# Kernel tuning notes

Hardware: AMD Instinct MI355X
Metric: run time of the kernel (lower is better)

The kernel has to match this reference:

```python
import jax, jax.numpy as jnp
import numpy as np

V, D, H, KVH, L, T_SEQ = 32000, 768, 12, 4, 6, 1024
HD = D // H          # 64
KVD = KVH * HD       # 256
B = 2
VE_LAYERS = [1, 3, 5]                 # has_ve(i, 6): i % 2 == 1
WINDOWS = [T_SEQ // 2, T_SEQ, T_SEQ // 2, T_SEQ, T_SEQ // 2, T_SEQ]  # 'SL' pattern, last forced L
SOFTCAP = 15.0


def _norm(x):
    # RMSNorm without learned scale, eps=1e-6, computed in fp32
    xf = x.astype(jnp.float32)
    return (xf * jax.lax.rsqrt(jnp.mean(jnp.square(xf), axis=-1, keepdims=True) + 1e-6)).astype(x.dtype)


def _rope(x, cos, sin):
    d = x.shape[3] // 2
    x1, x2 = x[..., :d], x[..., d:]
    return jnp.concatenate([x1 * cos + x2 * sin, -x1 * sin + x2 * cos], axis=3)


def _rotary_tables(T):
    ch = jnp.arange(0, HD, 2, dtype=jnp.float32)
    inv_freq = 1.0 / (10000.0 ** (ch / HD))
    t = jnp.arange(T, dtype=jnp.float32)
    freqs = jnp.outer(t, inv_freq)                 # [T, HD/2]
    cos = jnp.cos(freqs)[None, :, None, :]         # [1, T, 1, HD/2]
    sin = jnp.sin(freqs)[None, :, None, :]
    return cos, sin


def setup_inputs() -> dict:
    key = jax.random.key(0)
    ks = jax.random.split(key, 12)
    s = 0.02
    return {
        "idx": jax.random.randint(ks[0], (B, T_SEQ), 0, V, dtype=jnp.int64) if jax.config.read('jax_enable_x64') else jax.random.randint(ks[0], (B, T_SEQ), 0, V),
        "wte": jax.random.normal(ks[1], (V, D), jnp.float32) * s,
        "Wq": jax.random.normal(ks[2], (L, D, D), jnp.float32) * s,
        "Wk": jax.random.normal(ks[3], (L, KVD, D), jnp.float32) * s,
        "Wv": jax.random.normal(ks[4], (L, KVD, D), jnp.float32) * s,
        "Wo": jax.random.normal(ks[5], (L, D, D), jnp.float32) * s,
        "Wfc": jax.random.normal(ks[6], (L, 4 * D, D), jnp.float32) * s,
        "Wproj": jax.random.normal(ks[7], (L, D, 4 * D), jnp.float32) * s,
        "ve_tables": jax.random.normal(ks[8], (len(VE_LAYERS), V, KVD), jnp.float32) * s,
        "ve_gates": jax.random.normal(ks[9], (len(VE_LAYERS), KVH, 32), jnp.float32) * s,
        "resid_lambdas": jnp.ones((L,), jnp.float32),
        "x0_lambdas": jnp.zeros((L,), jnp.float32),
        "lm_head_w": jax.random.normal(ks[10], (V, D), jnp.float32) * s,
    }


def _attn(xn, idx, i, Wq, Wk, Wv, Wo, ve_tables, ve_gates, cos, sin, pos):
    Bsz, T, _ = xn.shape
    q = jnp.einsum('btc,dc->btd', xn, Wq[i]).reshape(Bsz, T, H, HD)
    k = jnp.einsum('btc,dc->btd', xn, Wk[i]).reshape(Bsz, T, KVH, HD)
    v = jnp.einsum('btc,dc->btd', xn, Wv[i]).reshape(Bsz, T, KVH, HD)
    if i in VE_LAYERS:
        j = VE_LAYERS.index(i)
        ve = ve_tables[j][idx].reshape(Bsz, T, KVH, HD)
        gate = 2.0 * jax.nn.sigmoid(jnp.einsum('btc,hc->bth', xn[..., :32], ve_gates[j]))
        v = v + gate[..., None] * ve
    q = _norm(_rope(q, cos, sin))
    k = _norm(_rope(k, cos, sin))
    # [B, heads, T, HD]
    q = q.transpose(0, 2, 1, 3)
    k = jnp.repeat(k.transpose(0, 2, 1, 3), H // KVH, axis=1)
    v = jnp.repeat(v.transpose(0, 2, 1, 3), H // KVH, axis=1)
    scores = jnp.einsum('bhqd,bhkd->bhqk', q, k) / np.sqrt(HD).astype(np.float32)
    w = WINDOWS[i]
    diff = pos[:, None] - pos[None, :]             # query - key
    mask = (diff >= 0) & (diff < w)                # w==T => plain causal
    scores = jnp.where(mask[None, None], scores, -jnp.inf)
    attn = jax.nn.softmax(scores, axis=-1)
    y = jnp.einsum('bhqk,bhkd->bhqd', attn, v)
    y = y.transpose(0, 2, 1, 3).reshape(Bsz, T, D)
    return jnp.einsum('btd,cd->btc', y, Wo[i])


def reference(idx, wte, Wq, Wk, Wv, Wo, Wfc, Wproj, ve_tables, ve_gates,
              resid_lambdas, x0_lambdas, lm_head_w):
    T = idx.shape[1]
    cos, sin = _rotary_tables(T)
    pos = jnp.arange(T)
    x = _norm(wte[idx])                            # [B, T, D]
    x0 = x
    for i in range(L):
        x = resid_lambdas[i] * x + x0_lambdas[i] * x0
        xn = _norm(x)
        x = x + _attn(xn, idx, i, Wq, Wk, Wv, Wo, ve_tables, ve_gates, cos, sin, pos)
        xn2 = _norm(x)
        h = jnp.square(jax.nn.relu(jnp.einsum('btc,fc->btf', xn2, Wfc[i])))
        x = x + jnp.einsum('btf,cf->btc', h, Wproj[i])
    x = _norm(x)
    logits = jnp.einsum('btd,vd->btv', x, lm_head_w).astype(jnp.float32)
    return SOFTCAP * jnp.tanh(logits / SOFTCAP)
```

## Files before the change

### kernel.cpp

```cpp
#include <hip/hip_runtime.h>
#include <math.h>

#define V_SZ   32000
#define D_SZ   768
#define H_N    12
#define KVH_N  4
#define L_N    6
#define T_SEQ  1024
#define HD_SZ  64
#define KVD_SZ 256
#define B_SZ   2
#define M_TOK  (B_SZ * T_SEQ)

typedef unsigned int u32;
typedef unsigned short u16;
typedef float f32x4 __attribute__((ext_vector_type(4)));
typedef short bf16x8 __attribute__((ext_vector_type(8)));
typedef u32 u32x4 __attribute__((ext_vector_type(4)));

__device__ __forceinline__ float block_reduce_sum_256(float v, float* ws4) {
#pragma unroll
  for (int o = 32; o; o >>= 1) v += __shfl_xor(v, o, 64);
  int wid = threadIdx.x >> 6;
  if ((threadIdx.x & 63) == 0) ws4[wid] = v;
  __syncthreads();
  return ws4[0] + ws4[1] + ws4[2] + ws4[3];
}

__global__ __launch_bounds__(256) void embed_norm_k(
    const int* __restrict__ idx, const float* __restrict__ wte,
    float* __restrict__ x, float* __restrict__ x0) {
  __shared__ float ws4[4];
  int bt = blockIdx.x;
  int tok = idx[bt];
  const float* row = wte + (size_t)tok * D_SZ;
  float v[3]; float ss = 0.f;
#pragma unroll
  for (int i = 0; i < 3; i++) { v[i] = row[threadIdx.x + i * 256]; ss += v[i] * v[i]; }
  ss = block_reduce_sum_256(ss, ws4);
  float r = rsqrtf(ss * (1.f / D_SZ) + 1e-6f);
  size_t base = (size_t)bt * D_SZ + threadIdx.x;
#pragma unroll
  for (int i = 0; i < 3; i++) {
    float o = v[i] * r;
    x[base + i * 256] = o;
    x0[base + i * 256] = o;
  }
}

__global__ __launch_bounds__(256) void resid_norm_k(
    float* __restrict__ x, const float* __restrict__ x0, float* __restrict__ xn,
    const float* __restrict__ rl, const float* __restrict__ xl, int layer) {
  __shared__ float ws4[4];
  int bt = blockIdx.x;
  float a = 1.f, b = 0.f;
  if (layer >= 0) { a = rl[layer]; b = xl[layer]; }
  size_t base = (size_t)bt * D_SZ + threadIdx.x;
  float v[3]; float ss = 0.f;
#pragma unroll
  for (int i = 0; i < 3; i++) {
    float nv = a * x[base + i * 256] + b * x0[base + i * 256];
    v[i] = nv; ss += nv * nv;
    if (layer >= 0) x[base + i * 256] = nv;
  }
  ss = block_reduce_sum_256(ss, ws4);
  float r = rsqrtf(ss * (1.f / D_SZ) + 1e-6f);
#pragma unroll
  for (int i = 0; i < 3; i++) xn[base + i * 256] = v[i] * r;
}

__global__ __launch_bounds__(64) void rope_norm_k(float* __restrict__ q, float* __restrict__ k) {
  int bt = blockIdx.x;
  int slot = blockIdx.y;
  int t = bt & (T_SEQ - 1);
  float* p;
  if (slot < H_N) p = q + (size_t)bt * D_SZ + slot * HD_SZ;
  else            p = k + (size_t)bt * KVD_SZ + (slot - H_N) * HD_SZ;
  int d = threadIdx.x;
  float self = p[d];
  float partner = p[d ^ 32];
  int j = d & 31;
  float inv = powf(10000.f, -(float)(2 * j) * (1.f / HD_SZ));
  float ang = (float)t * inv;
  float c = cosf(ang), s = sinf(ang);
  float out = (d < 32) ? (self * c + partner * s) : (self * c - partner * s);
  float ss = out * out;
#pragma unroll
  for (int o = 32; o; o >>= 1) ss += __shfl_xor(ss, o, 64);
  float r = rsqrtf(ss * (1.f / HD_SZ) + 1e-6f);
  p[d] = out * r;
}

__global__ __launch_bounds__(256) void ve_add_k(
    float* __restrict__ v, const float* __restrict__ xn, const int* __restrict__ idx,
    const float* __restrict__ vt, const float* __restrict__ vg) {
  int bt = blockIdx.x;
  int kh = threadIdx.x >> 6;
  const float* xr = xn + (size_t)bt * D_SZ;
  const float* gr = vg + kh * 32;
  float dot = 0.f;
#pragma unroll
  for (int c = 0; c < 32; c++) dot += xr[c] * gr[c];
  float g = 2.f / (1.f + expf(-dot));
  int tok = idx[bt];
  v[(size_t)bt * KVD_SZ + threadIdx.x] += g * vt[(size_t)tok * KVD_SZ + threadIdx.x];
}

#define QT 32
#define KT 64
__global__ __launch_bounds__(256) void attn_k(
    const float* __restrict__ qg, const float* __restrict__ kg,
    const float* __restrict__ vg, float* __restrict__ yg, int window) {
  __shared__ float Qs[QT][HD_SZ + 1];
  __shared__ float Ks[KT][HD_SZ + 1];
  __shared__ float Vs[KT][HD_SZ];
  __shared__ float S[QT][KT + 1];
  __shared__ float m_s[QT], l_s[QT], alpha_s[QT];

  int qt0 = blockIdx.x * QT;
  int h   = blockIdx.y;
  int b   = blockIdx.z;
  int kh  = h / (H_N / KVH_N);
  int tid = threadIdx.x;

  for (int e = tid; e < QT * HD_SZ; e += 256) {
    int qi = e >> 6, d = e & 63;
    Qs[qi][d] = qg[(size_t)(b * T_SEQ + qt0 + qi) * D_SZ + h * HD_SZ + d] * 0.125f;
  }
  if (tid < QT) { m_s[tid] = -INFINITY; l_s[tid] = 0.f; }

  int gq = tid >> 4;
  int tx = tid & 15;
  int qi0 = gq * 2;
  float o_acc[2][4] = {{0,0,0,0},{0,0,0,0}};

  int klo = qt0 - window + 1; if (klo < 0) klo = 0;
  int khi = qt0 + QT - 1;
  int kt_start = klo & ~(KT - 1);

  for (int kt = kt_start; kt <= khi; kt += KT) {
    __syncthreads();
    for (int e = tid; e < KT * HD_SZ; e += 256) {
      int kj = e >> 6, d = e & 63;
      size_t gidx = (size_t)(b * T_SEQ + kt + kj) * KVD_SZ + kh * HD_SZ + d;
      Ks[kj][d] = kg[gidx];
      Vs[kj][d] = vg[gidx];
    }
    __syncthreads();

    int kj0 = tx * 4;
    float sc[2][4] = {{0,0,0,0},{0,0,0,0}};
    for (int d = 0; d < HD_SZ; d++) {
      float a0 = Qs[qi0][d], a1 = Qs[qi0 + 1][d];
      float b0 = Ks[kj0][d], b1 = Ks[kj0 + 1][d], b2 = Ks[kj0 + 2][d], b3 = Ks[kj0 + 3][d];
      sc[0][0] += a0 * b0; sc[0][1] += a0 * b1; sc[0][2] += a0 * b2; sc[0][3] += a0 * b3;
      sc[1][0] += a1 * b0; sc[1][1] += a1 * b1; sc[1][2] += a1 * b2; sc[1][3] += a1 * b3;
    }
#pragma unroll
    for (int r = 0; r < 2; r++) {
      int qpos = qt0 + qi0 + r;
#pragma unroll
      for (int j = 0; j < 4; j++) {
        int diff = qpos - (kt + kj0 + j);
        if (diff < 0 || diff >= window) sc[r][j] = -INFINITY;
      }
    }
#pragma unroll
    for (int r = 0; r < 2; r++) {
      int row = qi0 + r;
      float m = fmaxf(fmaxf(sc[r][0], sc[r][1]), fmaxf(sc[r][2], sc[r][3]));
#pragma unroll
      for (int o = 1; o < 16; o <<= 1) m = fmaxf(m, __shfl_xor(m, o, 64));
      float m_old = m_s[row];
      float m_new = fmaxf(m_old, m);
      float alpha, psum = 0.f;
      if (m_new == -INFINITY) {
        alpha = 1.f;
#pragma unroll
        for (int j = 0; j < 4; j++) S[row][kj0 + j] = 0.f;
      } else {
        alpha = expf(m_old - m_new);
#pragma unroll
        for (int j = 0; j < 4; j++) {
          float p = expf(sc[r][j] - m_new);
          S[row][kj0 + j] = p;
          psum += p;
        }
      }
#pragma unroll
      for (int o = 1; o < 16; o <<= 1) psum += __shfl_xor(psum, o, 64);
      if (tx == 0) {
        m_s[row] = m_new;
        alpha_s[row] = alpha;
        l_s[row] = alpha * l_s[row] + psum;
      }
    }
    __syncthreads();

    int d0 = tx * 4;
#pragma unroll
    for (int r = 0; r < 2; r++) {
      float al = alpha_s[qi0 + r];
#pragma unroll
      for (int c = 0; c < 4; c++) o_acc[r][c] *= al;
    }
    for (int kj = 0; kj < KT; kj++) {
      float p0 = S[qi0][kj], p1 = S[qi0 + 1][kj];
      float v0 = Vs[kj][d0], v1 = Vs[kj][d0 + 1], v2 = Vs[kj][d0 + 2], v3 = Vs[kj][d0 + 3];
      o_acc[0][0] += p0 * v0; o_acc[0][1] += p0 * v1; o_acc[0][2] += p0 * v2; o_acc[0][3] += p0 * v3;
      o_acc[1][0] += p1 * v0; o_acc[1][1] += p1 * v1; o_acc[1][2] += p1 * v2; o_acc[1][3] += p1 * v3;
    }
  }

  int d0 = tx * 4;
#pragma unroll
  for (int r = 0; r < 2; r++) {
    float inv_l = 1.f / l_s[qi0 + r];
    size_t yi = (size_t)(b * T_SEQ + qt0 + qi0 + r) * D_SZ + h * HD_SZ + d0;
    yg[yi + 0] = o_acc[r][0] * inv_l;
    yg[yi + 1] = o_acc[r][1] * inv_l;
    yg[yi + 2] = o_acc[r][2] * inv_l;
    yg[yi + 3] = o_acc[r][3] * inv_l;
  }
}


__device__ __forceinline__ void split2(float a0, float a1, u32& hp, u32& lp) {
  u32 u0 = __float_as_uint(a0), u1 = __float_as_uint(a1);
  hp = (u0 >> 16) | (u1 & 0xffff0000u);
  float l0 = a0 - __uint_as_float(u0 & 0xffff0000u);
  float l1 = a1 - __uint_as_float(u1 & 0xffff0000u);
  u32 v0 = __float_as_uint(l0), v1 = __float_as_uint(l1);
  v0 += 0x7fffu + ((v0 >> 16) & 1u);
  v1 += 0x7fffu + ((v1 >> 16) & 1u);
  lp = (v0 >> 16) | (v1 & 0xffff0000u);
}

template <int BM, int EPI>
__global__ __launch_bounds__(256) void mfma_gemm_k(
    const float* __restrict__ X, const float* __restrict__ W, float* __restrict__ Y,
    int M, int N, int K) {
  constexpr int BN = 128;
  constexpr int BK = 32;
  constexpr int WM = BM / 2;
  constexpr int MR = WM / 16;
  constexpr int NR = 4;
  constexpr int ACH = BM * (BK / 8);
  constexpr int BCH = BN * (BK / 8);
  constexpr int TCH = ACH + BCH;
  constexpr int CPT = TCH / 256;
  static_assert(TCH % 256 == 0, "chunk count must divide evenly");
  static_assert(ACH % 256 == 0, "A/B chunk split must be wave-clean");

  __shared__ __align__(16) u16 sAh[ACH * 8], sAl[ACH * 8];
  __shared__ __align__(16) u16 sBh[BCH * 8], sBl[BCH * 8];

  const int tid  = threadIdx.x;
  const int lane = tid & 63;
  const int wave = tid >> 6;
  const int wr = wave >> 1, wc = wave & 1;
  const int l15 = lane & 15, l4 = lane >> 4;
  const int n0 = blockIdx.x * BN;
  const int m0 = blockIdx.y * BM;

  f32x4 acc[MR][NR];
#pragma unroll
  for (int mi = 0; mi < MR; mi++)
#pragma unroll
    for (int ni = 0; ni < NR; ni++) acc[mi][ni] = (f32x4){0.f, 0.f, 0.f, 0.f};

  const float* gsrc[CPT];
  int loff[CPT];
#pragma unroll
  for (int i = 0; i < CPT; i++) {
    int c = tid + i * 256;
    if ((i + 1) * 256 <= ACH) {
      int row = c >> 2, kc = c & 3;
      gsrc[i] = X + (size_t)(m0 + row) * K + kc * 8;
      loff[i] = (kc * BM + row) * 8;
    } else {
      int c2 = c - ACH;
      int row = c2 >> 2, kc = c2 & 3;
      gsrc[i] = W + (size_t)(n0 + row) * K + kc * 8;
      loff[i] = (kc * BN + row) * 8;
    }
  }

  float pre[CPT][8];
#pragma unroll
  for (int i = 0; i < CPT; i++) {
    *(float4*)&pre[i][0] = *(const float4*)(gsrc[i]);
    *(float4*)&pre[i][4] = *(const float4*)(gsrc[i] + 4);
  }

  const int nk = K / BK;
  for (int kt = 0; kt < nk; ++kt) {
    __syncthreads();
#pragma unroll
    for (int i = 0; i < CPT; i++) {
      u32 hp[4], lp[4];
#pragma unroll
      for (int j = 0; j < 4; j++)
        split2(pre[i][2 * j], pre[i][2 * j + 1], hp[j], lp[j]);
      bool ia = ((i + 1) * 256 <= ACH);
      u16* dh = ia ? sAh : sBh;
      u16* dl = ia ? sAl : sBl;
      *(u32x4*)(dh + loff[i]) = (u32x4){hp[0], hp[1], hp[2], hp[3]};
      *(u32x4*)(dl + loff[i]) = (u32x4){lp[0], lp[1], lp[2], lp[3]};
    }
    __syncthreads();

    if (kt + 1 < nk) {
#pragma unroll
      for (int i = 0; i < CPT; i++) {
        const float* p = gsrc[i] + (size_t)(kt + 1) * BK;
        *(float4*)&pre[i][0] = *(const float4*)(p);
        *(float4*)&pre[i][4] = *(const float4*)(p + 4);
      }
    }

    bf16x8 ah[MR], al[MR], bh[NR], bl[NR];
#pragma unroll
    for (int mi = 0; mi < MR; mi++) {
      int off = (l4 * BM + wr * WM + mi * 16 + l15) * 8;
      ah[mi] = *(const bf16x8*)(sAh + off);
      al[mi] = *(const bf16x8*)(sAl + off);
    }
#pragma unroll
    for (int ni = 0; ni < NR; ni++) {
      int off = (l4 * BN + wc * 64 + ni * 16 + l15) * 8;
      bh[ni] = *(const bf16x8*)(sBh + off);
      bl[ni] = *(const bf16x8*)(sBl + off);
    }
#pragma unroll
    for (int mi = 0; mi < MR; mi++)
#pragma unroll
      for (int ni = 0; ni < NR; ni++) {
        acc[mi][ni] = __builtin_amdgcn_mfma_f32_16x16x32_bf16(al[mi], bh[ni], acc[mi][ni], 0, 0, 0);
        acc[mi][ni] = __builtin_amdgcn_mfma_f32_16x16x32_bf16(ah[mi], bl[ni], acc[mi][ni], 0, 0, 0);
        acc[mi][ni] = __builtin_amdgcn_mfma_f32_16x16x32_bf16(ah[mi], bh[ni], acc[mi][ni], 0, 0, 0);
      }
  }

#pragma unroll
  for (int mi = 0; mi < MR; mi++) {
#pragma unroll
    for (int r = 0; r < 4; r++) {
      int grow = m0 + wr * WM + mi * 16 + l4 * 4 + r;
      size_t rowoff = (size_t)grow * N;
#pragma unroll
      for (int ni = 0; ni < NR; ni++) {
        int gcol = n0 + wc * 64 + ni * 16 + l15;
        float v = acc[mi][ni][r];
        float* yp = Y + rowoff + gcol;
        if (EPI == 1) v += *yp;
        else if (EPI == 2) { v = fmaxf(v, 0.f); v *= v; }
        else if (EPI == 3) v = 15.f * tanhf(v * (1.f / 15.f));
        *yp = v;
      }
    }
  }
}

extern "C" void kernel_launch(void* const* d_in, const int* in_sizes, int n_in,
                              void* d_out, int out_size, void* d_ws, size_t ws_size,
                              hipStream_t stream) {
  (void)in_sizes; (void)n_in; (void)out_size; (void)ws_size;
  const int*   idx = (const int*)d_in[0];
  const float* wte = (const float*)d_in[1];
  const float* Wq  = (const float*)d_in[2];
  const float* Wk  = (const float*)d_in[3];
  const float* Wv  = (const float*)d_in[4];
  const float* Wo  = (const float*)d_in[5];
  const float* Wfc = (const float*)d_in[6];
  const float* Wpr = (const float*)d_in[7];
  const float* vet = (const float*)d_in[8];
  const float* veg = (const float*)d_in[9];
  const float* rl  = (const float*)d_in[10];
  const float* xl  = (const float*)d_in[11];
  const float* lmw = (const float*)d_in[12];
  float* out = (float*)d_out;

  float* ws = (float*)d_ws;
  float* x    = ws;
  float* x0   = x  + (size_t)M_TOK * D_SZ;
  float* xn   = x0 + (size_t)M_TOK * D_SZ;
  float* q    = xn + (size_t)M_TOK * D_SZ;
  float* y    = q  + (size_t)M_TOK * D_SZ;
  float* kbuf = y  + (size_t)M_TOK * D_SZ;
  float* vbuf = kbuf + (size_t)M_TOK * KVD_SZ;
  float* hbuf = vbuf + (size_t)M_TOK * KVD_SZ;

  const int windows[L_N] = {T_SEQ / 2, T_SEQ, T_SEQ / 2, T_SEQ, T_SEQ / 2, T_SEQ};
  const int ve_map[L_N]  = {-1, 0, -1, 1, -1, 2};

  embed_norm_k<<<M_TOK, 256, 0, stream>>>(idx, wte, x, x0);

  for (int i = 0; i < L_N; i++) {
    resid_norm_k<<<M_TOK, 256, 0, stream>>>(x, x0, xn, rl, xl, i);

    mfma_gemm_k<64, 0><<<dim3(D_SZ / 128, M_TOK / 64), 256, 0, stream>>>(
        xn, Wq + (size_t)i * D_SZ * D_SZ, q, M_TOK, D_SZ, D_SZ);
    mfma_gemm_k<64, 0><<<dim3(KVD_SZ / 128, M_TOK / 64), 256, 0, stream>>>(
        xn, Wk + (size_t)i * KVD_SZ * D_SZ, kbuf, M_TOK, KVD_SZ, D_SZ);
    mfma_gemm_k<64, 0><<<dim3(KVD_SZ / 128, M_TOK / 64), 256, 0, stream>>>(
        xn, Wv + (size_t)i * KVD_SZ * D_SZ, vbuf, M_TOK, KVD_SZ, D_SZ);

    if (ve_map[i] >= 0) {
      ve_add_k<<<M_TOK, 256, 0, stream>>>(
          vbuf, xn, idx, vet + (size_t)ve_map[i] * V_SZ * KVD_SZ,
          veg + (size_t)ve_map[i] * KVH_N * 32);
    }

    rope_norm_k<<<dim3(M_TOK, H_N + KVH_N), 64, 0, stream>>>(q, kbuf);

    attn_k<<<dim3(T_SEQ / QT, H_N, B_SZ), 256, 0, stream>>>(q, kbuf, vbuf, y, windows[i]);

    mfma_gemm_k<64, 1><<<dim3(D_SZ / 128, M_TOK / 64), 256, 0, stream>>>(
        y, Wo + (size_t)i * D_SZ * D_SZ, x, M_TOK, D_SZ, D_SZ);

    resid_norm_k<<<M_TOK, 256, 0, stream>>>(x, x0, xn, rl, xl, -1);

    mfma_gemm_k<128, 2><<<dim3(4 * D_SZ / 128, M_TOK / 128), 256, 0, stream>>>(
        xn, Wfc + (size_t)i * 4 * D_SZ * D_SZ, hbuf, M_TOK, 4 * D_SZ, D_SZ);

    mfma_gemm_k<64, 1><<<dim3(D_SZ / 128, M_TOK / 64), 256, 0, stream>>>(
        hbuf, Wpr + (size_t)i * D_SZ * 4 * D_SZ, x, M_TOK, D_SZ, 4 * D_SZ);
  }

  resid_norm_k<<<M_TOK, 256, 0, stream>>>(x, x0, xn, rl, xl, -1);
  mfma_gemm_k<128, 3><<<dim3(V_SZ / 128, M_TOK / 128), 256, 0, stream>>>(
      xn, lmw, out, M_TOK, V_SZ, D_SZ);
}
```

Baseline: 3.671 ms.

## Pre-split activations into bf16 hi/lo in producers, fuse QKV GEMM, swizzle LDS

Producer kernels (resid_norm, attention, the FC GEMM epilogue) now write activations as separate bf16 high/low planes, so GEMMs load A tiles directly instead of converting fp32 each K-step. This halves nothing in bytes but removes per-tile split arithmetic on the A operand. The Q/K/V projections are merged into one launch over a 10-column grid, and the shared-memory layout uses an XOR swizzle to reduce bank conflicts. A small fp32 copy of the first 32 features is kept for the value-embedding gate.

After: 3.182 ms. 1.15x faster.

```diff
diff --git a/kernel.cpp b/kernel.cpp
--- a/kernel.cpp
+++ b/kernel.cpp
@@ -18,6 +18,26 @@
 typedef short bf16x8 __attribute__((ext_vector_type(8)));
 typedef u32 u32x4 __attribute__((ext_vector_type(4)));
 
+__device__ __forceinline__ void split2(float a0, float a1, u32& hp, u32& lp) {
+  u32 u0 = __float_as_uint(a0), u1 = __float_as_uint(a1);
+  hp = (u0 >> 16) | (u1 & 0xffff0000u);
+  float l0 = a0 - __uint_as_float(u0 & 0xffff0000u);
+  float l1 = a1 - __uint_as_float(u1 & 0xffff0000u);
+  u32 v0 = __float_as_uint(l0), v1 = __float_as_uint(l1);
+  v0 += 0x7fffu + ((v0 >> 16) & 1u);
+  v1 += 0x7fffu + ((v1 >> 16) & 1u);
+  lp = (v0 >> 16) | (v1 & 0xffff0000u);
+}
+
+__device__ __forceinline__ void split1(float a, u16& h, u16& l) {
+  u32 u = __float_as_uint(a);
+  h = (u16)(u >> 16);
+  float lo = a - __uint_as_float(u & 0xffff0000u);
+  u32 v = __float_as_uint(lo);
+  v += 0x7fffu + ((v >> 16) & 1u);
+  l = (u16)(v >> 16);
+}
+
 __device__ __forceinline__ float block_reduce_sum_256(float v, float* ws4) {
 #pragma unroll
   for (int o = 32; o; o >>= 1) v += __shfl_xor(v, o, 64);
@@ -49,7 +69,8 @@
 }
 
 __global__ __launch_bounds__(256) void resid_norm_k(
-    float* __restrict__ x, const float* __restrict__ x0, float* __restrict__ xn,
+    float* __restrict__ x, const float* __restrict__ x0,
+    u16* __restrict__ xnh, u16* __restrict__ xnl, float* __restrict__ xn32,
     const float* __restrict__ rl, const float* __restrict__ xl, int layer) {
   __shared__ float ws4[4];
   int bt = blockIdx.x;
@@ -66,7 +87,13 @@
   ss = block_reduce_sum_256(ss, ws4);
   float r = rsqrtf(ss * (1.f / D_SZ) + 1e-6f);
 #pragma unroll
-  for (int i = 0; i < 3; i++) xn[base + i * 256] = v[i] * r;
+  for (int i = 0; i < 3; i++) {
+    float o = v[i] * r;
+    u16 h, l; split1(o, h, l);
+    xnh[base + i * 256] = h;
+    xnl[base + i * 256] = l;
+  }
+  if (threadIdx.x < 32) xn32[(size_t)bt * 32 + threadIdx.x] = v[0] * r;
 }
 
 __global__ __launch_bounds__(64) void rope_norm_k(float* __restrict__ q, float* __restrict__ k) {
@@ -92,11 +119,11 @@
 }
 
 __global__ __launch_bounds__(256) void ve_add_k(
-    float* __restrict__ v, const float* __restrict__ xn, const int* __restrict__ idx,
+    float* __restrict__ v, const float* __restrict__ xn32, const int* __restrict__ idx,
     const float* __restrict__ vt, const float* __restrict__ vg) {
   int bt = blockIdx.x;
   int kh = threadIdx.x >> 6;
-  const float* xr = xn + (size_t)bt * D_SZ;
+  const float* xr = xn32 + (size_t)bt * 32;
   const float* gr = vg + kh * 32;
   float dot = 0.f;
 #pragma unroll
@@ -110,7 +137,7 @@
 #define KT 64
 __global__ __launch_bounds__(256) void attn_k(
     const float* __restrict__ qg, const float* __restrict__ kg,
-    const float* __restrict__ vg, float* __restrict__ yg, int window) {
+    const float* __restrict__ vg, u16* __restrict__ yh, u16* __restrict__ yl, int window) {
   __shared__ float Qs[QT][HD_SZ + 1];
   __shared__ float Ks[KT][HD_SZ + 1];
   __shared__ float Vs[KT][HD_SZ];
@@ -217,51 +244,39 @@
   for (int r = 0; r < 2; r++) {
     float inv_l = 1.f / l_s[qi0 + r];
     size_t yi = (size_t)(b * T_SEQ + qt0 + qi0 + r) * D_SZ + h * HD_SZ + d0;
-    yg[yi + 0] = o_acc[r][0] * inv_l;
-    yg[yi + 1] = o_acc[r][1] * inv_l;
-    yg[yi + 2] = o_acc[r][2] * inv_l;
-    yg[yi + 3] = o_acc[r][3] * inv_l;
-  }
-}
-
-
-__device__ __forceinline__ void split2(float a0, float a1, u32& hp, u32& lp) {
-  u32 u0 = __float_as_uint(a0), u1 = __float_as_uint(a1);
-  hp = (u0 >> 16) | (u1 & 0xffff0000u);
-  float l0 = a0 - __uint_as_float(u0 & 0xffff0000u);
-  float l1 = a1 - __uint_as_float(u1 & 0xffff0000u);
-  u32 v0 = __float_as_uint(l0), v1 = __float_as_uint(l1);
-  v0 += 0x7fffu + ((v0 >> 16) & 1u);
-  v1 += 0x7fffu + ((v1 >> 16) & 1u);
-  lp = (v0 >> 16) | (v1 & 0xffff0000u);
-}
+#pragma unroll
+    for (int c = 0; c < 4; c++) {
+      u16 hh_, ll_; split1(o_acc[r][c] * inv_l, hh_, ll_);
+      yh[yi + c] = hh_;
+      yl[yi + c] = ll_;
+    }
+  }
+}
+
 
 template <int BM, int EPI>
-__global__ __launch_bounds__(256) void mfma_gemm_k(
-    const float* __restrict__ X, const float* __restrict__ W, float* __restrict__ Y,
-    int M, int N, int K) {
+__device__ __forceinline__ void gemm_core(
+    const u16* __restrict__ Ah, const u16* __restrict__ Al,
+    const float* __restrict__ Wt,
+    float* __restrict__ Yt,
+    u16* __restrict__ Yth, u16* __restrict__ Ytl,
+    int ldY, int K, int m0) {
   constexpr int BN = 128;
   constexpr int BK = 32;
   constexpr int WM = BM / 2;
   constexpr int MR = WM / 16;
   constexpr int NR = 4;
-  constexpr int ACH = BM * (BK / 8);
-  constexpr int BCH = BN * (BK / 8);
-  constexpr int TCH = ACH + BCH;
-  constexpr int CPT = TCH / 256;
-  static_assert(TCH % 256 == 0, "chunk count must divide evenly");
-  static_assert(ACH % 256 == 0, "A/B chunk split must be wave-clean");
-
-  __shared__ __align__(16) u16 sAh[ACH * 8], sAl[ACH * 8];
-  __shared__ __align__(16) u16 sBh[BCH * 8], sBl[BCH * 8];
-
-  const int tid  = threadIdx.x;
-  const int lane = tid & 63;
-  const int wave = tid >> 6;
+  constexpr int AGT = BM * 4 / 256;
+  constexpr int BGT = BN * 4 / 256;
+  static_assert(BM * 4 % 256 == 0, "");
+
+  __shared__ __align__(16) u16 sAh[BM * 32], sAl[BM * 32];
+  __shared__ __align__(16) u16 sBh[BN * 32], sBl[BN * 32];
+
+  const int tid = threadIdx.x;
+  const int lane = tid & 63, wave = tid >> 6;
   const int wr = wave >> 1, wc = wave & 1;
   const int l15 = lane & 15, l4 = lane >> 4;
-  const int n0 = blockIdx.x * BN;
-  const int m0 = blockIdx.y * BM;
 
   f32x4 acc[MR][NR];
 #pragma unroll
@@ -269,76 +284,90 @@
 #pragma unroll
     for (int ni = 0; ni < NR; ni++) acc[mi][ni] = (f32x4){0.f, 0.f, 0.f, 0.f};
 
-  const float* gsrc[CPT];
-  int loff[CPT];
-#pragma unroll
-  for (int i = 0; i < CPT; i++) {
+  const u16 *agh[AGT], *agl[AGT];
+  int aoff[AGT];
+#pragma unroll
+  for (int i = 0; i < AGT; i++) {
     int c = tid + i * 256;
-    if ((i + 1) * 256 <= ACH) {
-      int row = c >> 2, kc = c & 3;
-      gsrc[i] = X + (size_t)(m0 + row) * K + kc * 8;
-      loff[i] = (kc * BM + row) * 8;
-    } else {
-      int c2 = c - ACH;
-      int row = c2 >> 2, kc = c2 & 3;
-      gsrc[i] = W + (size_t)(n0 + row) * K + kc * 8;
-      loff[i] = (kc * BN + row) * 8;
-    }
-  }
-
-  float pre[CPT][8];
-#pragma unroll
-  for (int i = 0; i < CPT; i++) {
-    *(float4*)&pre[i][0] = *(const float4*)(gsrc[i]);
-    *(float4*)&pre[i][4] = *(const float4*)(gsrc[i] + 4);
+    int row = c >> 2, kc = c & 3;
+    agh[i] = Ah + (size_t)(m0 + row) * K + kc * 8;
+    agl[i] = Al + (size_t)(m0 + row) * K + kc * 8;
+    aoff[i] = ((row * 4 + kc) ^ (row & 7)) * 8;
+  }
+  const float* bg[BGT];
+  int boff[BGT];
+#pragma unroll
+  for (int i = 0; i < BGT; i++) {
+    int c = tid + i * 256;
+    int row = c >> 2, kc = c & 3;
+    bg[i] = Wt + (size_t)row * K + kc * 8;
+    boff[i] = ((row * 4 + kc) ^ (row & 7)) * 8;
+  }
+
+  u32x4 pAh[AGT], pAl[AGT];
+  float pB[BGT][8];
+#pragma unroll
+  for (int i = 0; i < AGT; i++) { pAh[i] = *(const u32x4*)agh[i]; pAl[i] = *(const u32x4*)agl[i]; }
+#pragma unroll
+  for (int i = 0; i < BGT; i++) {
+    *(float4*)&pB[i][0] = *(const float4*)bg[i];
+    *(float4*)&pB[i][4] = *(const float4*)(bg[i] + 4);
   }
 
   const int nk = K / BK;
   for (int kt = 0; kt < nk; ++kt) {
     __syncthreads();
 #pragma unroll
-    for (int i = 0; i < CPT; i++) {
+    for (int i = 0; i < AGT; i++) {
+      *(u32x4*)(sAh + aoff[i]) = pAh[i];
+      *(u32x4*)(sAl + aoff[i]) = pAl[i];
+    }
+#pragma unroll
+    for (int i = 0; i < BGT; i++) {
       u32 hp[4], lp[4];
 #pragma unroll
-      for (int j = 0; j < 4; j++)
-        split2(pre[i][2 * j], pre[i][2 * j + 1], hp[j], lp[j]);
-      bool ia = ((i + 1) * 256 <= ACH);
-      u16* dh = ia ? sAh : sBh;
-      u16* dl = ia ? sAl : sBl;
-      *(u32x4*)(dh + loff[i]) = (u32x4){hp[0], hp[1], hp[2], hp[3]};
-      *(u32x4*)(dl + loff[i]) = (u32x4){lp[0], lp[1], lp[2], lp[3]};
+      for (int j = 0; j < 4; j++) split2(pB[i][2 * j], pB[i][2 * j + 1], hp[j], lp[j]);
+      *(u32x4*)(sBh + boff[i]) = (u32x4){hp[0], hp[1], hp[2], hp[3]};
+      *(u32x4*)(sBl + boff[i]) = (u32x4){lp[0], lp[1], lp[2], lp[3]};
     }
     __syncthreads();
 
     if (kt + 1 < nk) {
 #pragma unroll
-      for (int i = 0; i < CPT; i++) {
-        const float* p = gsrc[i] + (size_t)(kt + 1) * BK;
-        *(float4*)&pre[i][0] = *(const float4*)(p);
-        *(float4*)&pre[i][4] = *(const float4*)(p + 4);
-      }
-    }
-
-    bf16x8 ah[MR], al[MR], bh[NR], bl[NR];
+      for (int i = 0; i < AGT; i++) {
+        pAh[i] = *(const u32x4*)(agh[i] + (size_t)(kt + 1) * BK);
+        pAl[i] = *(const u32x4*)(agl[i] + (size_t)(kt + 1) * BK);
+      }
+#pragma unroll
+      for (int i = 0; i < BGT; i++) {
+        const float* p = bg[i] + (size_t)(kt + 1) * BK;
+        *(float4*)&pB[i][0] = *(const float4*)p;
+        *(float4*)&pB[i][4] = *(const float4*)(p + 4);
+      }
+    }
+
+    bf16x8 fah[MR], fal[MR], fbh[NR], fbl[NR];
 #pragma unroll
     for (int mi = 0; mi < MR; mi++) {
-      int off = (l4 * BM + wr * WM + mi * 16 + l15) * 8;
-      ah[mi] = *(const bf16x8*)(sAh + off);
-      al[mi] = *(const bf16x8*)(sAl + off);
+      int row = wr * WM + mi * 16 + l15;
+      int off = ((row * 4 + l4) ^ (row & 7)) * 8;
+      fah[mi] = *(const bf16x8*)(sAh + off);
+      fal[mi] = *(const bf16x8*)(sAl + off);
     }
 #pragma unroll
     for (int ni = 0; ni < NR; ni++) {
-      int off = (l4 * BN + wc * 64 + ni * 16 + l15) * 8;
-      bh[ni] = *(const bf16x8*)(sBh + off);
-      bl[ni] = *(const bf16x8*)(sBl + off);
+      int row = wc * 64 + ni * 16 + l15;
+      int off = ((row * 4 + l4) ^ (row & 7)) * 8;
+      fbh[ni] = *(const bf16x8*)(sBh + off);
+      fbl[ni] = *(const bf16x8*)(sBl + off);
     }
 #pragma unroll
     for (int mi = 0; mi < MR; mi++)
 #pragma unroll
       for (int ni = 0; ni < NR; ni++) {
-        acc[mi][ni] = __builtin_amdgcn_mfma_f32_16x16x32_bf16(al[mi], bh[ni], acc[mi][ni], 0, 0, 0);
-        acc[mi][ni] = __builtin_amdgcn_mfma_f32_16x16x32_bf16(ah[mi], bl[ni], acc[mi][ni], 0, 0, 0);
-        acc[mi][ni] = __builtin_amdgcn_mfma_f32_16x16x32_bf16(ah[mi], bh[ni], acc[mi][ni], 0, 0, 0);
+        acc[mi][ni] = __builtin_amdgcn_mfma_f32_16x16x32_bf16(fal[mi], fbh[ni], acc[mi][ni], 0, 0, 0);
+        acc[mi][ni] = __builtin_amdgcn_mfma_f32_16x16x32_bf16(fah[mi], fbl[ni], acc[mi][ni], 0, 0, 0);
+        acc[mi][ni] = __builtin_amdgcn_mfma_f32_16x16x32_bf16(fah[mi], fbh[ni], acc[mi][ni], 0, 0, 0);
       }
   }
 
@@ -347,19 +376,51 @@
 #pragma unroll
     for (int r = 0; r < 4; r++) {
       int grow = m0 + wr * WM + mi * 16 + l4 * 4 + r;
-      size_t rowoff = (size_t)grow * N;
+      size_t rowoff = (size_t)grow * ldY;
 #pragma unroll
       for (int ni = 0; ni < NR; ni++) {
-        int gcol = n0 + wc * 64 + ni * 16 + l15;
+        int col = wc * 64 + ni * 16 + l15;
         float v = acc[mi][ni][r];
-        float* yp = Y + rowoff + gcol;
-        if (EPI == 1) v += *yp;
-        else if (EPI == 2) { v = fmaxf(v, 0.f); v *= v; }
-        else if (EPI == 3) v = 15.f * tanhf(v * (1.f / 15.f));
-        *yp = v;
-      }
-    }
-  }
+        size_t oidx = rowoff + col;
+        if (EPI == 0) {
+          Yt[oidx] = v;
+        } else if (EPI == 1) {
+          Yt[oidx] += v;
+        } else if (EPI == 2) {
+          v = fmaxf(v, 0.f); v *= v;
+          u16 h, l; split1(v, h, l);
+          Yth[oidx] = h; Ytl[oidx] = l;
+        } else {
+          Yt[oidx] = 15.f * tanhf(v * (1.f / 15.f));
+        }
+      }
+    }
+  }
+}
+
+template <int BM, int EPI>
+__global__ __launch_bounds__(256) void mfma_gemm_k(
+    const u16* __restrict__ Ah, const u16* __restrict__ Al,
+    const float* __restrict__ W, float* __restrict__ Y,
+    u16* __restrict__ Yh, u16* __restrict__ Yl,
+    int N, int K) {
+  int n0 = blockIdx.x * 128;
+  gemm_core<BM, EPI>(Ah, Al, W + (size_t)n0 * K,
+                     Y ? Y + n0 : nullptr,
+                     Yh ? Yh + n0 : nullptr, Yl ? Yl + n0 : nullptr,
+                     N, K, blockIdx.y * BM);
+}
+
+__global__ __launch_bounds__(256) void qkv_gemm_k(
+    const u16* __restrict__ Ah, const u16* __restrict__ Al,
+    const float* __restrict__ Wq, const float* __restrict__ Wk, const float* __restrict__ Wv,
+    float* __restrict__ q, float* __restrict__ kb, float* __restrict__ vb) {
+  int t = blockIdx.x;
+  const float* W; float* Y; int ldY;
+  if (t < 6)      { W = Wq + (size_t)t * 128 * D_SZ;       Y = q  + t * 128;       ldY = D_SZ; }
+  else if (t < 8) { W = Wk + (size_t)(t - 6) * 128 * D_SZ; Y = kb + (t - 6) * 128; ldY = KVD_SZ; }
+  else            { W = Wv + (size_t)(t - 8) * 128 * D_SZ; Y = vb + (t - 8) * 128; ldY = KVD_SZ; }
+  gemm_core<64, 0>(Ah, Al, W, Y, nullptr, nullptr, ldY, D_SZ, blockIdx.y * 64);
 }
 
 extern "C" void kernel_launch(void* const* d_in, const int* in_sizes, int n_in,
@@ -383,13 +444,17 @@
 
   float* ws = (float*)d_ws;
   float* x    = ws;
-  float* x0   = x  + (size_t)M_TOK * D_SZ;
-  float* xn   = x0 + (size_t)M_TOK * D_SZ;
-  float* q    = xn + (size_t)M_TOK * D_SZ;
-  float* y    = q  + (size_t)M_TOK * D_SZ;
-  float* kbuf = y  + (size_t)M_TOK * D_SZ;
+  float* x0   = x    + (size_t)M_TOK * D_SZ;
+  float* q    = x0   + (size_t)M_TOK * D_SZ;
+  float* kbuf = q    + (size_t)M_TOK * D_SZ;
   float* vbuf = kbuf + (size_t)M_TOK * KVD_SZ;
-  float* hbuf = vbuf + (size_t)M_TOK * KVD_SZ;
+  float* xn32 = vbuf + (size_t)M_TOK * KVD_SZ;
+  u16* xnh = (u16*)(xn32 + (size_t)M_TOK * 32);
+  u16* xnl = xnh + (size_t)M_TOK * D_SZ;
+  u16* hh  = xnl + (size_t)M_TOK * D_SZ;
+  u16* hl  = hh  + (size_t)M_TOK * 4 * D_SZ;
+  u16* yh  = hh;
+  u16* yl  = hl;
 
   const int windows[L_N] = {T_SEQ / 2, T_SEQ, T_SEQ / 2, T_SEQ, T_SEQ / 2, T_SEQ};
   const int ve_map[L_N]  = {-1, 0, -1, 1, -1, 2};
@@ -397,38 +462,36 @@
   embed_norm_k<<<M_TOK, 256, 0, stream>>>(idx, wte, x, x0);
 
   for (int i = 0; i < L_N; i++) {
-    resid_norm_k<<<M_TOK, 256, 0, stream>>>(x, x0, xn, rl, xl, i);
-
-    mfma_gemm_k<64, 0><<<dim3(D_SZ / 128, M_TOK / 64), 256, 0, stream>>>(
-        xn, Wq + (size_t)i * D_SZ * D_SZ, q, M_TOK, D_SZ, D_SZ);
-    mfma_gemm_k<64, 0><<<dim3(KVD_SZ / 128, M_TOK / 64), 256, 0, stream>>>(
-        xn, Wk + (size_t)i * KVD_SZ * D_SZ, kbuf, M_TOK, KVD_SZ, D_SZ);
-    mfma_gemm_k<64, 0><<<dim3(KVD_SZ / 128, M_TOK / 64), 256, 0, stream>>>(
-        xn, Wv + (size_t)i * KVD_SZ * D_SZ, vbuf, M_TOK, KVD_SZ, D_SZ);
+    resid_norm_k<<<M_TOK, 256, 0, stream>>>(x, x0, xnh, xnl, xn32, rl, xl, i);
+
+    qkv_gemm_k<<<dim3(10, M_TOK / 64), 256, 0, stream>>>(
+        xnh, xnl,
+        Wq + (size_t)i * D_SZ * D_SZ, Wk + (size_t)i * KVD_SZ * D_SZ,
+        Wv + (size_t)i * KVD_SZ * D_SZ, q, kbuf, vbuf);
 
     if (ve_map[i] >= 0) {
       ve_add_k<<<M_TOK, 256, 0, stream>>>(
-          vbuf, xn, idx, vet + (size_t)ve_map[i] * V_SZ * KVD_SZ,
+          vbuf, xn32, idx, vet + (size_t)ve_map[i] * V_SZ * KVD_SZ,
           veg + (size_t)ve_map[i] * KVH_N * 32);
     }
 
     rope_norm_k<<<dim3(M_TOK, H_N + KVH_N), 64, 0, stream>>>(q, kbuf);
 
-    attn_k<<<dim3(T_SEQ / QT, H_N, B_SZ), 256, 0, stream>>>(q, kbuf, vbuf, y, windows[i]);
+    attn_k<<<dim3(T_SEQ / QT, H_N, B_SZ), 256, 0, stream>>>(q, kbuf, vbuf, yh, yl, windows[i]);
 
     mfma_gemm_k<64, 1><<<dim3(D_SZ / 128, M_TOK / 64), 256, 0, stream>>>(
-        y, Wo + (size_t)i * D_SZ * D_SZ, x, M_TOK, D_SZ, D_SZ);
-
-    resid_norm_k<<<M_TOK, 256, 0, stream>>>(x, x0, xn, rl, xl, -1);
+        yh, yl, Wo + (size_t)i * D_SZ * D_SZ, x, nullptr, nullptr, D_SZ, D_SZ);
+
+    resid_norm_k<<<M_TOK, 256, 0, stream>>>(x, x0, xnh, xnl, xn32, rl, xl, -1);
 
     mfma_gemm_k<128, 2><<<dim3(4 * D_SZ / 128, M_TOK / 128), 256, 0, stream>>>(
-        xn, Wfc + (size_t)i * 4 * D_SZ * D_SZ, hbuf, M_TOK, 4 * D_SZ, D_SZ);
+        xnh, xnl, Wfc + (size_t)i * 4 * D_SZ * D_SZ, nullptr, hh, hl, 4 * D_SZ, D_SZ);
 
     mfma_gemm_k<64, 1><<<dim3(D_SZ / 128, M_TOK / 64), 256, 0, stream>>>(
-        hbuf, Wpr + (size_t)i * D_SZ * 4 * D_SZ, x, M_TOK, D_SZ, 4 * D_SZ);
-  }
-
-  resid_norm_k<<<M_TOK, 256, 0, stream>>>(x, x0, xn, rl, xl, -1);
+        hh, hl, Wpr + (size_t)i * D_SZ * 4 * D_SZ, x, nullptr, nullptr, D_SZ, 4 * D_SZ);
+  }
+
+  resid_norm_k<<<M_TOK, 256, 0, stream>>>(x, x0, xnh, xnl, xn32, rl, xl, -1);
   mfma_gemm_k<128, 3><<<dim3(V_SZ / 128, M_TOK / 128), 256, 0, stream>>>(
-      xn, lmw, out, M_TOK, V_SZ, D_SZ);
-}
+      xnh, xnl, lmw, out, nullptr, nullptr, V_SZ, D_SZ);
+}
```
